# Optimization experiments

Measured on AMD Instinct MI355X. Metric: run time of the kernel, lower is better.

## Reference

```python
import math
import jax, jax.numpy as jnp
import numpy as np

N = 1600; C_IN = 16; HID = 64; OUT = 64; D_K = 8; N_HEADS = 8
CUTS = 8; NUM_RBF = 8; RBF_PROJ = 4; RADIUS = 6.0; ALPHA = 3.0

def leaky(x):
    return jnp.where(x >= 0, x, 0.2 * x)

def group_norm(x, gamma, beta, groups=4, eps=1e-5):
    # x: [N, C]; torch GroupNorm applied on [1, C, N]: stats over (C/groups, N) per group
    n, c = x.shape
    xg = x.T.reshape(groups, -1)
    mu = jnp.mean(xg, axis=1, keepdims=True)
    var = jnp.mean((xg - mu) ** 2, axis=1, keepdims=True)
    xn = ((xg - mu) * jax.lax.rsqrt(var + eps)).reshape(c, n).T
    return xn * gamma + beta

def setup_inputs():
    key = jax.random.key(0)
    ks = jax.random.split(key, 32)
    def rn(k, shape, s=0.1):
        return (jax.random.normal(k, shape) * s).astype(jnp.float32)
    return {
        "points": jax.random.normal(ks[0], (N, 3), jnp.float32),
        "nuv": jax.random.normal(ks[1], (N, 3, 3), jnp.float32),
        "features": jax.random.normal(ks[2], (N, C_IN), jnp.float32),
        "w_in1": rn(ks[3], (HID, C_IN)), "b_in1": rn(ks[4], (HID,)),
        "w_in2": rn(ks[5], (HID, HID)), "b_in2": rn(ks[6], (HID,)),
        "g_in": 1.0 + rn(ks[7], (HID,)), "be_in": rn(ks[8], (HID,)),
        "wq": rn(ks[9], (HID, HID)), "bq": rn(ks[10], (HID,)),
        "wk": rn(ks[11], (HID, HID)), "bk": rn(ks[12], (HID,)),
        "wv": rn(ks[13], (HID, HID)), "bv": rn(ks[14], (HID,)),
        "conv_w1": rn(ks[15], (CUTS, 4 + RBF_PROJ), 0.5),
        "conv_b1": jnp.abs(rn(ks[16], (CUTS,), 0.5)),
        "conv_w2": rn(ks[17], (HID, CUTS), 0.3), "conv_b2": rn(ks[18], (HID,), 0.3),
        "rbf_log_sigma": jnp.log(jnp.asarray(0.6 * 2.0 / (NUM_RBF - 1), jnp.float32)),
        "rbf_a": rn(ks[19], (RBF_PROJ, NUM_RBF), 0.3), "rbf_b": rn(ks[20], (RBF_PROJ,), 0.1),
        "rbf_centers": jnp.linspace(0.0, 2.0, NUM_RBF, dtype=jnp.float32),
        "w_o1": rn(ks[21], (OUT, HID)), "b_o1": rn(ks[22], (OUT,)),
        "w_o2": rn(ks[23], (OUT, OUT)), "b_o2": rn(ks[24], (OUT,)),
        "g_out": 1.0 + rn(ks[25], (OUT,)), "be_out": rn(ks[26], (OUT,)),
        "w_res": rn(ks[27], (OUT, C_IN)), "b_res": rn(ks[28], (OUT,)),
    }

def reference(points, nuv, features, w_in1, b_in1, w_in2, b_in2, g_in, be_in,
              wq, bq, wk, bk, wv, bv, conv_w1, conv_b1, conv_w2, conv_b2,
              rbf_log_sigma, rbf_a, rbf_b, rbf_centers,
              w_o1, b_o1, w_o2, b_o2, g_out, be_out, w_res, b_res):
    # point-wise MLP + GroupNorm
    h = leaky(features @ w_in1.T + b_in1)
    h = leaky(h @ w_in2.T + b_in2)
    h = group_norm(h, g_in, be_in)
    Q = h @ wq.T + bq
    K = h @ wk.T + bk
    V = h @ wv.T + bv
    pts = points / (math.sqrt(2.0) * RADIUS)
    diff = pts[None, :, :] - pts[:, None, :]            # [N, N, 3] = x_j - x_i
    n_i = nuv[:, 0, :]
    n_j = jax.lax.stop_gradient(n_i)                    # j-side normals are detached in the original
    ndot = jnp.einsum("ia,ja->ij", n_i, n_j)            # <n_i, n_j>
    d2 = jnp.sum(diff ** 2, axis=-1) * (2.0 - ndot) ** 2  # pseudo-geodesic squared distance
    W = (1.0 + d2 / ALPHA) ** (-ALPHA)                  # geodesic window weight
    d2_safe = jnp.where(d2 > 0, d2, 1.0)
    base_d = jnp.where(d2 > 0, jnp.sqrt(d2_safe), 0.0)  # safe sqrt (finite grad at 0)
    sigma = jnp.maximum(jnp.exp(rbf_log_sigma), 1e-6)
    R = jnp.exp(-((base_d[:, :, None] - rbf_centers) ** 2) / (2.0 * sigma ** 2))  # [N,N,NUM_RBF]
    R_proj = R @ rbf_a.T + rbf_b                        # [N, N, RBF_PROJ]
    X_loc = jnp.einsum("iab,ijb->ija", nuv, diff)       # local tangent-frame coords [N,N,3]
    X = jnp.concatenate([X_loc, ndot[:, :, None], R_proj], axis=-1)  # [N, N, 4+RBF_PROJ]
    F1 = jax.nn.relu(X @ conv_w1.T + conv_b1)           # shared conv layer-1 [N, N, CUTS]
    scale = 1.0 / math.sqrt(D_K)
    heads = []
    for h_id in range(N_HEADS):
        s = slice(h_id * D_K, (h_id + 1) * D_K)
        Fh = jax.nn.relu(F1 @ conv_w2[s].T + conv_b2[s])      # per-head conv weights [N, N, D_K]
        S = (Q[:, s] @ K[:, s].T) * scale                     # attention logits [N, N]
        P = jax.nn.softmax(S, axis=1) * W                     # softmax over j, fused with window
        heads.append(jnp.einsum("ij,ijc,jc->ic", P, Fh, V[:, s]))
    agg = jnp.concatenate(heads, axis=1)                      # [N, HID]
    o = leaky(agg @ w_o1.T + b_o1)
    o = leaky(o @ w_o2.T + b_o2)
    o = group_norm(o, g_out, be_out)
    return o + features @ w_res.T + b_res
```

## Files before the change

kernel.cpp:

```cpp
#include <hip/hip_runtime.h>

typedef __fp16 h2 __attribute__((ext_vector_type(2)));
typedef unsigned int u32;
typedef unsigned short u16;

#define NPTS 1600
#define NCHUNK 10
#define CHUNKJ 160
#define TILE 32
#define QS (0.35355339059327373f*1.4426950408889634f)
#define PSCALE 0.11785113019775793f
#define LOG2E 1.4426950408889634f

__device__ __forceinline__ float leaky(float x){ return x >= 0.f ? x : 0.2f*x; }
__device__ __forceinline__ float d4(float4 a, float4 b){ return a.x*b.x + a.y*b.y + a.z*b.z + a.w*b.w; }
__device__ __forceinline__ u32 pkn(float a, float b){ h2 v; v[0]=(__fp16)a; v[1]=(__fp16)b; return __builtin_bit_cast(u32,v); }
__device__ __forceinline__ h2 u2h(u32 u){ return __builtin_bit_cast(h2,u); }
__device__ __forceinline__ float dot2(h2 a, h2 b, float c){ return __builtin_amdgcn_fdot2(a,b,c,false); }
__device__ __forceinline__ u32 rfl(u32 x){ return (u32)__builtin_amdgcn_readfirstlane((int)x); }

__global__ __launch_bounds__(256) void k_in(
    const float* __restrict__ feat, const float* __restrict__ w1, const float* __restrict__ b1,
    const float* __restrict__ w2, const float* __restrict__ b2,
    const float* __restrict__ conv_w1, const float* __restrict__ conv_b1,
    const float* __restrict__ conv_w2,
    const float* __restrict__ rbf_a, const float* __restrict__ rbf_b,
    const float* __restrict__ rbf_ls, const float* __restrict__ rbf_c,
    float* __restrict__ h2out, float* __restrict__ bstat1, float* __restrict__ wpk)
{
  __shared__ float sh[4][64];
  __shared__ float sred[4][8];
  int t = threadIdx.x, w = t>>6, c = t&63;
  int i = blockIdx.x*4 + w;

  if (blockIdx.x == 0) {
    u32* wp = (u32*)wpk;
    {
      int row = t>>2, q = t&3;
      wp[32 + row*4 + q] = pkn(conv_w2[row*8+2*q], conv_w2[row*8+2*q+1]);
    }
    if (t < 32) {
      int cc = t>>2, kq = t&3;
      float a0=0.f, a1=0.f;
      #pragma unroll
      for (int p=0;p<4;p++){ a0 += conv_w1[cc*8+4+p]*rbf_a[p*8+2*kq]; a1 += conv_w1[cc*8+4+p]*rbf_a[p*8+2*kq+1]; }
      wp[cc*4+kq] = pkn(a0,a1);
    } else if (t < 40) {
      int cc = t-32; float s = conv_b1[cc];
      #pragma unroll
      for (int p=0;p<4;p++) s += conv_w1[cc*8+4+p]*rbf_b[p];
      wpk[288+cc] = s;
    } else if (t == 40) {
      float sig = fmaxf(expf(rbf_ls[0]), 1e-6f);
      float m = -LOG2E/(2.f*sig*sig);
      float c0 = rbf_c[0];
      float dl = rbf_c[1] - rbf_c[0];
      wpk[296] = c0;
      wpk[297] = m;
      wpk[298] = -2.f*m*dl;
      wpk[299] = m*dl*dl;
    }
  }

  const float4* f4 = (const float4*)(feat + i*16);
  float4 f0=f4[0], f1v=f4[1], f2v=f4[2], f3v=f4[3];
  const float4* w1r = (const float4*)(w1 + c*16);
  float h1 = b1[c] + d4(f0,w1r[0]) + d4(f1v,w1r[1]) + d4(f2v,w1r[2]) + d4(f3v,w1r[3]);
  h1 = leaky(h1);
  sh[w][c] = h1;
  __syncthreads();
  float hh = b2[c];
  #pragma unroll
  for (int k4=0;k4<16;k4++){
    float4 hv = *(const float4*)&sh[w][k4*4];
    hh += d4(hv, *(const float4*)&w2[c*64 + k4*4]);
  }
  hh = leaky(hh);
  h2out[i*64+c] = hh;

  float s = hh, qq = hh*hh;
  s += __shfl_xor(s,1);  qq += __shfl_xor(qq,1);
  s += __shfl_xor(s,2);  qq += __shfl_xor(qq,2);
  s += __shfl_xor(s,4);  qq += __shfl_xor(qq,4);
  s += __shfl_xor(s,8);  qq += __shfl_xor(qq,8);
  if ((c&15)==0){ int g=c>>4; sred[w][g]=s; sred[w][4+g]=qq; }
  __syncthreads();
  if (t<8) bstat1[blockIdx.x*8+t] = sred[0][t]+sred[1][t]+sred[2][t]+sred[3][t];
}

__global__ __launch_bounds__(256) void k_qkv(
  const float* __restrict__ h2b, const float* __restrict__ bstat1,
  const float* __restrict__ g_in, const float* __restrict__ be_in,
  const float* __restrict__ wq, const float* __restrict__ bq,
  const float* __restrict__ wk, const float* __restrict__ bk,
  const float* __restrict__ wv, const float* __restrict__ bv,
  const float* __restrict__ pts, const float* __restrict__ nuv,
  u32* __restrict__ Q16, u32* __restrict__ K16, u32* __restrict__ V16,
  float* __restrict__ PN)
{
  __shared__ float sh[4][64];
  __shared__ float sp[64];
  __shared__ float sst[8];
  int t=threadIdx.x, w=t>>6, c=t&63;
  int i = blockIdx.x*4 + w;
  if (t<64){ int g=t&7; float s=0.f;
    for (int m=t>>3; m<400; m+=8) s += bstat1[m*8+g];
    sp[t]=s; }
  __syncthreads();
  if (t<8){ float s=0.f;
    #pragma unroll
    for (int q=0;q<8;q++) s += sp[q*8+t];
    sst[t]=s; }
  __syncthreads();
  int g = c>>4;
  const float inv = 1.f/25600.f;
  float mu = sst[g]*inv;
  float var = sst[4+g]*inv - mu*mu;
  float rs = rsqrtf(var + 1e-5f);
  float hn = (h2b[i*64+c]-mu)*rs*g_in[c] + be_in[c];
  sh[w][c] = hn;
  __syncthreads();
  float q=bq[c], k=bk[c], v=bv[c];
  #pragma unroll
  for (int k4=0;k4<16;k4++){
    float4 hv = *(const float4*)&sh[w][k4*4];
    q += d4(hv, *(const float4*)&wq[c*64+k4*4]);
    k += d4(hv, *(const float4*)&wk[c*64+k4*4]);
    v += d4(hv, *(const float4*)&wv[c*64+k4*4]);
  }
  u16* Q16u = (u16*)Q16;
  u16* K16u = (u16*)K16;
  u16* V16u = (u16*)V16;
  __fp16 qh = (__fp16)(q*QS);
  __fp16 kh = (__fp16)k;
  __fp16 vh = (__fp16)v;
  Q16u[i*64 + c] = __builtin_bit_cast(u16, qh);
  K16u[i*64 + c] = __builtin_bit_cast(u16, kh);
  int pr = ((i>>5)<<4) + (i&15);
  int hf = (i>>4)&1;
  V16u[(pr*64 + c)*2 + hf] = __builtin_bit_cast(u16, vh);
  if (c < 6){
    float pv = (c<3) ? pts[i*3+c]*PSCALE : nuv[i*9+(c-3)];
    PN[i*8+c] = pv;
  } else if (c < 8) PN[i*8+c] = 0.f;
}

__global__ __launch_bounds__(256) void k_pair(
  const u32* __restrict__ Q16, const u32* __restrict__ K16, const u32* __restrict__ V16,
  const float* __restrict__ PN, const float* __restrict__ nuv,
  const float* __restrict__ w1, const float* __restrict__ wpk,
  const float* __restrict__ b2g, float* __restrict__ part)
{
  __shared__ __align__(16) float SM[4608];
  u32*   sQ16 = (u32*)SM;
  u32*   sWX  = (u32*)SM + 576;
  float* sRed = SM;

  int t = threadIdx.x;
  int r = t & 15, jl = t >> 4;
  int bx = blockIdx.x;
  int rb = bx % 100, jc = bx / 100;
  int I0 = rb*16, J0 = jc*CHUNKJ;
  int i = I0 + r;

  if (t < 128) {
    int qrow = t>>3, qq4 = (t&7)<<2;
    *(uint4*)&sQ16[qrow*36+qq4] = *(const uint4*)&Q16[(I0+qrow)*32+qq4];
  }
  if (t < 128) {
    int r2 = t>>3, cc = t&7, ib = (I0+r2)*9;
    float a0=w1[cc*8], a1=w1[cc*8+1], a2=w1[cc*8+2];
    float x = a0*nuv[ib+0] + a1*nuv[ib+3] + a2*nuv[ib+6];
    float y = a0*nuv[ib+1] + a1*nuv[ib+4] + a2*nuv[ib+7];
    float z = a0*nuv[ib+2] + a1*nuv[ib+5] + a2*nuv[ib+8];
    sWX[r2*20+cc*2+0] = pkn(x,y);
    sWX[r2*20+cc*2+1] = pkn(z, w1[cc*8+3]);
  }
  __syncthreads();
  u32 wxp[16];
  #pragma unroll
  for (int q2=0;q2<4;q2++) *(uint4*)&wxp[q2*4] = *(const uint4*)&sWX[r*20+q2*4];

  const u32* wp = (const u32*)wpk;
  h2 wr[8][4];
  #pragma unroll
  for (int cc=0;cc<8;cc++)
    #pragma unroll
    for (int q2=0;q2<4;q2++) wr[cc][q2] = u2h(rfl(wp[cc*4+q2]));
  const u32* w2p = wp + 32;
  const float* b1p = wpk + 288;
  float c0  = wpk[296];
  float mco = wpk[297];
  float C2  = wpk[298];
  float A1  = wpk[299];

  float4 pni0 = *(const float4*)&PN[i*8];
  float4 pni1 = *(const float4*)&PN[i*8+4];
  float pix = pni0.x, piy = pni0.y, piz = pni0.z;
  float nix = pni0.w, niy = pni1.x, niz = pni1.y;

  float acc[64];
  #pragma unroll
  for (int o=0;o<64;o++) acc[o] = 0.f;
  float lh[8];
  #pragma unroll
  for (int h=0;h<8;h++) lh[h] = 0.f;

  #pragma unroll 1
  for (int tb=0; tb<CHUNKJ; tb+=TILE) {
    int jbase = J0 + tb;
    int jA = jbase + jl;
    int jB = jA + 16;

    h2 F1p[2][4];
    float Wv[2];
    #pragma unroll
    for (int jj=0;jj<2;jj++) {
      int j = jj ? jB : jA;
      float4 a0 = *(const float4*)&PN[j*8];
      float4 a1 = *(const float4*)&PN[j*8+4];
      float dx = a0.x-pix, dy = a0.y-piy, dz = a0.z-piz;
      float ndot = nix*a0.w + niy*a1.x + niz*a1.y;
      float d2r = dx*dx + dy*dy + dz*dz;
      float wf = 2.f - ndot;
      float d2 = d2r*wf*wf;
      float tp = fmaf(d2, 0.3333333333333333f, 1.f);
      Wv[jj] = __builtin_amdgcn_rcpf(tp*tp*tp);
      float dd = __builtin_amdgcn_sqrtf(d2);
      float g0 = dd - c0;
      float s2 = mco*g0*g0;
      float uu = C2*g0;
      float R[8];
      #pragma unroll
      for (int k=0;k<8;k++){
        float kf = (float)k, k2f = (float)(k*k);
        R[k] = __builtin_amdgcn_exp2f(fmaf(kf, uu, fmaf(k2f, A1, s2)));
      }
      h2 xv0; xv0[0]=(__fp16)dx; xv0[1]=(__fp16)dy;
      h2 xv1; xv1[0]=(__fp16)dz; xv1[1]=(__fp16)ndot;
      h2 r01=__builtin_amdgcn_cvt_pkrtz(R[0],R[1]);
      h2 r23=__builtin_amdgcn_cvt_pkrtz(R[2],R[3]);
      h2 r45=__builtin_amdgcn_cvt_pkrtz(R[4],R[5]);
      h2 r67=__builtin_amdgcn_cvt_pkrtz(R[6],R[7]);
      float F1f[8];
      #pragma unroll
      for (int cc=0;cc<8;cc++){
        float f = dot2(r67, wr[cc][3], b1p[cc]);
        f = dot2(r45, wr[cc][2], f);
        f = dot2(r23, wr[cc][1], f);
        f = dot2(r01, wr[cc][0], f);
        f = dot2(u2h(wxp[cc*2+1]), xv1, f);
        f = dot2(u2h(wxp[cc*2+0]), xv0, f);
        F1f[cc] = fmaxf(f, 0.f);
      }
      F1p[jj][0]=__builtin_amdgcn_cvt_pkrtz(F1f[0],F1f[1]);
      F1p[jj][1]=__builtin_amdgcn_cvt_pkrtz(F1f[2],F1f[3]);
      F1p[jj][2]=__builtin_amdgcn_cvt_pkrtz(F1f[4],F1f[5]);
      F1p[jj][3]=__builtin_amdgcn_cvt_pkrtz(F1f[6],F1f[7]);
    }
    h2 Wvp = __builtin_amdgcn_cvt_pkrtz(Wv[0], Wv[1]);

    const u32* kArow = &K16[jA*32];
    const u32* kBrow = &K16[jB*32];
    const u32* vrow  = &V16[(((u32)jbase>>1)+jl)*64];

    #pragma unroll
    for (int h=0;h<8;h++) {
      uint4 qh = *(const uint4*)&sQ16[r*36 + (h<<2)];
      uint4 kA = *(const uint4*)&kArow[h<<2];
      uint4 kB = *(const uint4*)&kBrow[h<<2];
      float S0 = dot2(u2h(qh.x),u2h(kA.x), dot2(u2h(qh.y),u2h(kA.y),
                 dot2(u2h(qh.z),u2h(kA.z), dot2(u2h(qh.w),u2h(kA.w), 0.f))));
      float S1 = dot2(u2h(qh.x),u2h(kB.x), dot2(u2h(qh.y),u2h(kB.y),
                 dot2(u2h(qh.z),u2h(kB.z), dot2(u2h(qh.w),u2h(kB.w), 0.f))));
      float e0 = __builtin_amdgcn_exp2f(S0);
      float e1 = __builtin_amdgcn_exp2f(S1);
      lh[h] += e0 + e1;
      h2 ewp = __builtin_amdgcn_cvt_pkrtz(e0,e1) * Wvp;
      uint4 vpA = *(const uint4*)&vrow[h*8];
      uint4 vpB = *(const uint4*)&vrow[h*8+4];
      u32 vparr[8] = {vpA.x,vpA.y,vpA.z,vpA.w,vpB.x,vpB.y,vpB.z,vpB.w};
      #pragma unroll
      for (int cc=0;cc<8;cc++){
        int rw = h*8+cc;
        h2 w0=u2h(w2p[rw*4+0]), w1h=u2h(w2p[rw*4+1]), w2h=u2h(w2p[rw*4+2]), w3h=u2h(w2p[rw*4+3]);
        float b2v = b2g[rw];
        float fh0 = dot2(F1p[0][0],w0, dot2(F1p[0][1],w1h, dot2(F1p[0][2],w2h, dot2(F1p[0][3],w3h, b2v))));
        float fh1 = dot2(F1p[1][0],w0, dot2(F1p[1][1],w1h, dot2(F1p[1][2],w2h, dot2(F1p[1][3],w3h, b2v))));
        h2 fhp = __builtin_amdgcn_cvt_pkrtz(fmaxf(fh0,0.f), fmaxf(fh1,0.f));
        h2 ev = u2h(vparr[cc]) * ewp;
        acc[rw] = dot2(fhp, ev, acc[rw]);
      }
    }
  }

  #pragma unroll
  for (int o=0;o<64;o++){ acc[o] += __shfl_xor(acc[o],16); acc[o] += __shfl_xor(acc[o],32); }
  #pragma unroll
  for (int h=0;h<8;h++){ lh[h] += __shfl_xor(lh[h],16); lh[h] += __shfl_xor(lh[h],32); }
  __syncthreads();
  int wv = t >> 6, lane = t & 63;
  if (lane < 16) {
    #pragma unroll
    for (int o=0;o<64;o++) sRed[(wv*16+lane)*72+o] = acc[o];
    #pragma unroll
    for (int h=0;h<8;h++) sRed[(wv*16+lane)*72+64+h] = lh[h];
  }
  __syncthreads();
  for (int v2 = t; v2 < 16*72; v2 += 256) {
    int rr = v2/72, o = v2 - rr*72;
    part[(jc*NPTS + I0 + rr)*72 + o] =
      sRed[(0*16+rr)*72+o] + sRed[(1*16+rr)*72+o] + sRed[(2*16+rr)*72+o] + sRed[(3*16+rr)*72+o];
  }
}

__global__ __launch_bounds__(256) void k_agg(
  const float* __restrict__ part, const float* __restrict__ w_o1, const float* __restrict__ b_o1,
  const float* __restrict__ w_o2, const float* __restrict__ b_o2,
  float* __restrict__ o2b, float* __restrict__ bstat2)
{
  __shared__ float sh[4][64];
  __shared__ float sred[4][8];
  int t = threadIdx.x, w = t>>6, c = t&63;
  int i = blockIdx.x*4 + w;
  int h = c>>3;
  float a = 0.f, L = 0.f;
  #pragma unroll
  for (int jc=0;jc<NCHUNK;jc++){
    const float* p = part + (jc*NPTS + i)*72;
    a += p[c]; L += p[64+h];
  }
  float agg = a / L;
  sh[w][c] = agg; __syncthreads();
  float o1 = b_o1[c];
  #pragma unroll
  for (int k4=0;k4<16;k4++){
    float4 hv = *(const float4*)&sh[w][k4*4];
    o1 += d4(hv, *(const float4*)&w_o1[c*64+k4*4]);
  }
  o1 = leaky(o1);
  __syncthreads();
  sh[w][c] = o1; __syncthreads();
  float o2 = b_o2[c];
  #pragma unroll
  for (int k4=0;k4<16;k4++){
    float4 hv = *(const float4*)&sh[w][k4*4];
    o2 += d4(hv, *(const float4*)&w_o2[c*64+k4*4]);
  }
  o2 = leaky(o2);
  o2b[i*64+c] = o2;

  float s = o2, qq = o2*o2;
  s += __shfl_xor(s,1);  qq += __shfl_xor(qq,1);
  s += __shfl_xor(s,2);  qq += __shfl_xor(qq,2);
  s += __shfl_xor(s,4);  qq += __shfl_xor(qq,4);
  s += __shfl_xor(s,8);  qq += __shfl_xor(qq,8);
  if ((c&15)==0){ int g=c>>4; sred[w][g]=s; sred[w][4+g]=qq; }
  __syncthreads();
  if (t<8) bstat2[blockIdx.x*8+t] = sred[0][t]+sred[1][t]+sred[2][t]+sred[3][t];
}

__global__ __launch_bounds__(256) void k_out(
  const float* __restrict__ o2b, const float* __restrict__ bstat2,
  const float* __restrict__ g_out, const float* __restrict__ be_out,
  const float* __restrict__ feat, const float* __restrict__ w_res, const float* __restrict__ b_res,
  float* __restrict__ out)
{
  __shared__ float sp[64];
  __shared__ float sst[8];
  int t = threadIdx.x, w = t>>6, c = t&63;
  int i = blockIdx.x*4 + w;
  if (t<64){ int g=t&7; float s=0.f;
    for (int m=t>>3; m<400; m+=8) s += bstat2[m*8+g];
    sp[t]=s; }
  __syncthreads();
  if (t<8){ float s=0.f;
    #pragma unroll
    for (int q=0;q<8;q++) s += sp[q*8+t];
    sst[t]=s; }
  __syncthreads();
  int g = c>>4;
  const float inv = 1.f/25600.f;
  float mu = sst[g]*inv;
  float var = sst[4+g]*inv - mu*mu;
  float rs = rsqrtf(var + 1e-5f);
  float on = (o2b[i*64+c]-mu)*rs*g_out[c] + be_out[c];
  const float4* f4 = (const float4*)(feat + i*16);
  const float4* wr = (const float4*)(w_res + c*16);
  float res = b_res[c] + d4(f4[0],wr[0]) + d4(f4[1],wr[1]) + d4(f4[2],wr[2]) + d4(f4[3],wr[3]);
  out[i*64+c] = on + res;
}

extern "C" void kernel_launch(void* const* d_in, const int* in_sizes, int n_in,
                              void* d_out, int out_size, void* d_ws, size_t ws_size,
                              hipStream_t stream) {
  const float* points  = (const float*)d_in[0];
  const float* nuv     = (const float*)d_in[1];
  const float* feat    = (const float*)d_in[2];
  const float* w_in1   = (const float*)d_in[3];
  const float* b_in1   = (const float*)d_in[4];
  const float* w_in2   = (const float*)d_in[5];
  const float* b_in2   = (const float*)d_in[6];
  const float* g_in    = (const float*)d_in[7];
  const float* be_in   = (const float*)d_in[8];
  const float* wq      = (const float*)d_in[9];
  const float* bq      = (const float*)d_in[10];
  const float* wk      = (const float*)d_in[11];
  const float* bk      = (const float*)d_in[12];
  const float* wv      = (const float*)d_in[13];
  const float* bv      = (const float*)d_in[14];
  const float* conv_w1 = (const float*)d_in[15];
  const float* conv_b1 = (const float*)d_in[16];
  const float* conv_w2 = (const float*)d_in[17];
  const float* conv_b2 = (const float*)d_in[18];
  const float* rbf_ls  = (const float*)d_in[19];
  const float* rbf_a   = (const float*)d_in[20];
  const float* rbf_b   = (const float*)d_in[21];
  const float* rbf_c   = (const float*)d_in[22];
  const float* w_o1    = (const float*)d_in[23];
  const float* b_o1    = (const float*)d_in[24];
  const float* w_o2    = (const float*)d_in[25];
  const float* b_o2    = (const float*)d_in[26];
  const float* g_out   = (const float*)d_in[27];
  const float* be_out  = (const float*)d_in[28];
  const float* w_res   = (const float*)d_in[29];
  const float* b_res   = (const float*)d_in[30];

  float* ws     = (float*)d_ws;
  float* h2f    = ws;
  u32*   Q16    = (u32*)(ws + 102400);
  u32*   K16    = (u32*)(ws + 153600);
  u32*   V16    = (u32*)(ws + 204800);
  float* PN     = ws + 256000;
  float* bstat1 = ws + 268800;
  float* bstat2 = ws + 272000;
  float* wpk    = ws + 275200;
  float* part   = ws + 275520;
  float* o2b    = ws + 1427520;
  float* out    = (float*)d_out;

  k_in<<<400, 256, 0, stream>>>(feat, w_in1, b_in1, w_in2, b_in2,
                                conv_w1, conv_b1, conv_w2, rbf_a, rbf_b, rbf_ls, rbf_c,
                                h2f, bstat1, wpk);
  k_qkv<<<400, 256, 0, stream>>>(h2f, bstat1, g_in, be_in, wq, bq, wk, bk, wv, bv,
                                 points, nuv, Q16, K16, V16, PN);
  k_pair<<<1000, 256, 0, stream>>>(Q16, K16, V16, PN, nuv, conv_w1, wpk, conv_b2, part);
  k_agg<<<400, 256, 0, stream>>>(part, w_o1, b_o1, w_o2, b_o2, o2b, bstat2);
  k_out<<<400, 256, 0, stream>>>(o2b, bstat2, g_out, be_out, feat, w_res, b_res, out);
}
```

Before: 238.1 us.

## Split pair kernel into two head-halves and compute RBF by recurrence

The pair kernel now processes heads in two passes of four, halving the per-thread accumulator array to cut register pressure and raise occupancy. The cost is recomputing the geometric and conv layer-1 features for each pass. The eight RBF exponentials are replaced by two exp2 calls plus a multiplicative recurrence, using constants precomputed in the setup kernel. Dot-product chains are split into parallel partial sums for more instruction-level parallelism, and the WX weights are read from shared memory instead of being held in registers.

```diff
diff --git a/kernel.cpp b/kernel.cpp
--- a/kernel.cpp
+++ b/kernel.cpp
@@ -55,10 +55,14 @@
       float m = -LOG2E/(2.f*sig*sig);
       float c0 = rbf_c[0];
       float dl = rbf_c[1] - rbf_c[0];
+      float A1v = m*dl*dl;
       wpk[296] = c0;
       wpk[297] = m;
       wpk[298] = -2.f*m*dl;
-      wpk[299] = m*dl*dl;
+      wpk[299] = A1v;
+      float Av = exp2f(A1v);
+      wpk[300] = Av;
+      wpk[301] = Av*Av;
     }
   }
 
@@ -151,10 +155,9 @@
   const float* __restrict__ w1, const float* __restrict__ wpk,
   const float* __restrict__ b2g, float* __restrict__ part)
 {
-  __shared__ __align__(16) float SM[4608];
-  u32*   sQ16 = (u32*)SM;
-  u32*   sWX  = (u32*)SM + 576;
-  float* sRed = SM;
+  __shared__ __align__(16) u32   sQ16[16*36];
+  __shared__ __align__(16) u32   sWX[16*20];
+  __shared__ __align__(16) float sRedH[4*16*36];
 
   int t = threadIdx.x;
   int r = t & 15, jl = t >> 4;
@@ -177,9 +180,6 @@
     sWX[r2*20+cc*2+1] = pkn(z, w1[cc*8+3]);
   }
   __syncthreads();
-  u32 wxp[16];
-  #pragma unroll
-  for (int q2=0;q2<4;q2++) *(uint4*)&wxp[q2*4] = *(const uint4*)&sWX[r*20+q2*4];
 
   const u32* wp = (const u32*)wpk;
   h2 wr[8][4];
@@ -192,125 +192,128 @@
   float c0  = wpk[296];
   float mco = wpk[297];
   float C2  = wpk[298];
-  float A1  = wpk[299];
+  float Af  = wpk[300];
+  float A2f = wpk[301];
 
   float4 pni0 = *(const float4*)&PN[i*8];
   float4 pni1 = *(const float4*)&PN[i*8+4];
   float pix = pni0.x, piy = pni0.y, piz = pni0.z;
   float nix = pni0.w, niy = pni1.x, niz = pni1.y;
 
-  float acc[64];
-  #pragma unroll
-  for (int o=0;o<64;o++) acc[o] = 0.f;
-  float lh[8];
-  #pragma unroll
-  for (int h=0;h<8;h++) lh[h] = 0.f;
-
   #pragma unroll 1
-  for (int tb=0; tb<CHUNKJ; tb+=TILE) {
-    int jbase = J0 + tb;
-    int jA = jbase + jl;
-    int jB = jA + 16;
-
-    h2 F1p[2][4];
-    float Wv[2];
-    #pragma unroll
-    for (int jj=0;jj<2;jj++) {
-      int j = jj ? jB : jA;
-      float4 a0 = *(const float4*)&PN[j*8];
-      float4 a1 = *(const float4*)&PN[j*8+4];
-      float dx = a0.x-pix, dy = a0.y-piy, dz = a0.z-piz;
-      float ndot = nix*a0.w + niy*a1.x + niz*a1.y;
-      float d2r = dx*dx + dy*dy + dz*dz;
-      float wf = 2.f - ndot;
-      float d2 = d2r*wf*wf;
-      float tp = fmaf(d2, 0.3333333333333333f, 1.f);
-      Wv[jj] = __builtin_amdgcn_rcpf(tp*tp*tp);
-      float dd = __builtin_amdgcn_sqrtf(d2);
-      float g0 = dd - c0;
-      float s2 = mco*g0*g0;
-      float uu = C2*g0;
-      float R[8];
-      #pragma unroll
-      for (int k=0;k<8;k++){
-        float kf = (float)k, k2f = (float)(k*k);
-        R[k] = __builtin_amdgcn_exp2f(fmaf(kf, uu, fmaf(k2f, A1, s2)));
+  for (int hp=0; hp<2; hp++) {
+    float acc[32];
+    #pragma unroll
+    for (int o=0;o<32;o++) acc[o] = 0.f;
+    float lh[4] = {0.f,0.f,0.f,0.f};
+
+    #pragma unroll 1
+    for (int tb=0; tb<CHUNKJ; tb+=TILE) {
+      int jbase = J0 + tb;
+      int jA = jbase + jl;
+      int jB = jA + 16;
+
+      h2 F1p[2][4];
+      float Wv[2];
+      #pragma unroll
+      for (int jj=0;jj<2;jj++) {
+        int j = jj ? jB : jA;
+        float4 a0 = *(const float4*)&PN[j*8];
+        float4 a1 = *(const float4*)&PN[j*8+4];
+        float dx = a0.x-pix, dy = a0.y-piy, dz = a0.z-piz;
+        float ndot = nix*a0.w + niy*a1.x + niz*a1.y;
+        float d2r = dx*dx + dy*dy + dz*dz;
+        float wf = 2.f - ndot;
+        float d2 = d2r*wf*wf;
+        float tp = fmaf(d2, 0.3333333333333333f, 1.f);
+        Wv[jj] = __builtin_amdgcn_rcpf(tp*tp*tp);
+        float dd = __builtin_amdgcn_sqrtf(d2);
+        float g0 = dd - c0;
+        float E = __builtin_amdgcn_exp2f(mco*g0*g0);
+        float U = __builtin_amdgcn_exp2f(C2*g0);
+        float R[8];
+        R[0] = E;
+        float tt = U*Af;
+        #pragma unroll
+        for (int k=1;k<8;k++){ R[k] = R[k-1]*tt; tt *= A2f; }
+        h2 xv0; xv0[0]=(__fp16)dx; xv0[1]=(__fp16)dy;
+        h2 xv1; xv1[0]=(__fp16)dz; xv1[1]=(__fp16)ndot;
+        h2 r01=__builtin_amdgcn_cvt_pkrtz(R[0],R[1]);
+        h2 r23=__builtin_amdgcn_cvt_pkrtz(R[2],R[3]);
+        h2 r45=__builtin_amdgcn_cvt_pkrtz(R[4],R[5]);
+        h2 r67=__builtin_amdgcn_cvt_pkrtz(R[6],R[7]);
+        float F1f[8];
+        #pragma unroll
+        for (int cc=0;cc<8;cc++){
+          uint2 wx2 = *(const uint2*)&sWX[r*20+cc*2];
+          float fa = dot2(r01, wr[cc][0], dot2(r23, wr[cc][1], b1p[cc]));
+          float fb = dot2(r45, wr[cc][2], dot2(r67, wr[cc][3], 0.f));
+          float fc = dot2(u2h(wx2.x), xv0, dot2(u2h(wx2.y), xv1, 0.f));
+          F1f[cc] = fmaxf(fa+fb+fc, 0.f);
+        }
+        F1p[jj][0]=__builtin_amdgcn_cvt_pkrtz(F1f[0],F1f[1]);
+        F1p[jj][1]=__builtin_amdgcn_cvt_pkrtz(F1f[2],F1f[3]);
+        F1p[jj][2]=__builtin_amdgcn_cvt_pkrtz(F1f[4],F1f[5]);
+        F1p[jj][3]=__builtin_amdgcn_cvt_pkrtz(F1f[6],F1f[7]);
       }
-      h2 xv0; xv0[0]=(__fp16)dx; xv0[1]=(__fp16)dy;
-      h2 xv1; xv1[0]=(__fp16)dz; xv1[1]=(__fp16)ndot;
-      h2 r01=__builtin_amdgcn_cvt_pkrtz(R[0],R[1]);
-      h2 r23=__builtin_amdgcn_cvt_pkrtz(R[2],R[3]);
-      h2 r45=__builtin_amdgcn_cvt_pkrtz(R[4],R[5]);
-      h2 r67=__builtin_amdgcn_cvt_pkrtz(R[6],R[7]);
-      float F1f[8];
-      #pragma unroll
-      for (int cc=0;cc<8;cc++){
-        float f = dot2(r67, wr[cc][3], b1p[cc]);
-        f = dot2(r45, wr[cc][2], f);
-        f = dot2(r23, wr[cc][1], f);
-        f = dot2(r01, wr[cc][0], f);
-        f = dot2(u2h(wxp[cc*2+1]), xv1, f);
-        f = dot2(u2h(wxp[cc*2+0]), xv0, f);
-        F1f[cc] = fmaxf(f, 0.f);
-      }
-      F1p[jj][0]=__builtin_amdgcn_cvt_pkrtz(F1f[0],F1f[1]);
-      F1p[jj][1]=__builtin_amdgcn_cvt_pkrtz(F1f[2],F1f[3]);
-      F1p[jj][2]=__builtin_amdgcn_cvt_pkrtz(F1f[4],F1f[5]);
-      F1p[jj][3]=__builtin_amdgcn_cvt_pkrtz(F1f[6],F1f[7]);
-    }
-    h2 Wvp = __builtin_amdgcn_cvt_pkrtz(Wv[0], Wv[1]);
-
-    const u32* kArow = &K16[jA*32];
-    const u32* kBrow = &K16[jB*32];
-    const u32* vrow  = &V16[(((u32)jbase>>1)+jl)*64];
-
-    #pragma unroll
-    for (int h=0;h<8;h++) {
-      uint4 qh = *(const uint4*)&sQ16[r*36 + (h<<2)];
-      uint4 kA = *(const uint4*)&kArow[h<<2];
-      uint4 kB = *(const uint4*)&kBrow[h<<2];
-      float S0 = dot2(u2h(qh.x),u2h(kA.x), dot2(u2h(qh.y),u2h(kA.y),
-                 dot2(u2h(qh.z),u2h(kA.z), dot2(u2h(qh.w),u2h(kA.w), 0.f))));
-      float S1 = dot2(u2h(qh.x),u2h(kB.x), dot2(u2h(qh.y),u2h(kB.y),
-                 dot2(u2h(qh.z),u2h(kB.z), dot2(u2h(qh.w),u2h(kB.w), 0.f))));
-      float e0 = __builtin_amdgcn_exp2f(S0);
-      float e1 = __builtin_amdgcn_exp2f(S1);
-      lh[h] += e0 + e1;
-      h2 ewp = __builtin_amdgcn_cvt_pkrtz(e0,e1) * Wvp;
-      uint4 vpA = *(const uint4*)&vrow[h*8];
-      uint4 vpB = *(const uint4*)&vrow[h*8+4];
-      u32 vparr[8] = {vpA.x,vpA.y,vpA.z,vpA.w,vpB.x,vpB.y,vpB.z,vpB.w};
-      #pragma unroll
-      for (int cc=0;cc<8;cc++){
-        int rw = h*8+cc;
-        h2 w0=u2h(w2p[rw*4+0]), w1h=u2h(w2p[rw*4+1]), w2h=u2h(w2p[rw*4+2]), w3h=u2h(w2p[rw*4+3]);
-        float b2v = b2g[rw];
-        float fh0 = dot2(F1p[0][0],w0, dot2(F1p[0][1],w1h, dot2(F1p[0][2],w2h, dot2(F1p[0][3],w3h, b2v))));
-        float fh1 = dot2(F1p[1][0],w0, dot2(F1p[1][1],w1h, dot2(F1p[1][2],w2h, dot2(F1p[1][3],w3h, b2v))));
-        h2 fhp = __builtin_amdgcn_cvt_pkrtz(fmaxf(fh0,0.f), fmaxf(fh1,0.f));
-        h2 ev = u2h(vparr[cc]) * ewp;
-        acc[rw] = dot2(fhp, ev, acc[rw]);
+      h2 Wvp = __builtin_amdgcn_cvt_pkrtz(Wv[0], Wv[1]);
+
+      const u32* kArow = &K16[jA*32];
+      const u32* kBrow = &K16[jB*32];
+      const u32* vrow  = &V16[(((u32)jbase>>1)+jl)*64];
+
+      #pragma unroll
+      for (int hh=0; hh<4; hh++) {
+        int h = (hp<<2) + hh;
+        uint4 qh = *(const uint4*)&sQ16[r*36 + (h<<2)];
+        uint4 kA = *(const uint4*)&kArow[h<<2];
+        uint4 kB = *(const uint4*)&kBrow[h<<2];
+        float S0 = dot2(u2h(qh.x),u2h(kA.x), dot2(u2h(qh.y),u2h(kA.y), 0.f))
+                 + dot2(u2h(qh.z),u2h(kA.z), dot2(u2h(qh.w),u2h(kA.w), 0.f));
+        float S1 = dot2(u2h(qh.x),u2h(kB.x), dot2(u2h(qh.y),u2h(kB.y), 0.f))
+                 + dot2(u2h(qh.z),u2h(kB.z), dot2(u2h(qh.w),u2h(kB.w), 0.f));
+        float e0 = __builtin_amdgcn_exp2f(S0);
+        float e1 = __builtin_amdgcn_exp2f(S1);
+        lh[hh] += e0 + e1;
+        h2 ewp = __builtin_amdgcn_cvt_pkrtz(e0,e1) * Wvp;
+        uint4 vpA = *(const uint4*)&vrow[h*8];
+        uint4 vpB = *(const uint4*)&vrow[h*8+4];
+        u32 vparr[8] = {vpA.x,vpA.y,vpA.z,vpA.w,vpB.x,vpB.y,vpB.z,vpB.w};
+        #pragma unroll
+        for (int cc=0;cc<8;cc++){
+          int rw = h*8+cc;
+          h2 w0=u2h(w2p[rw*4+0]), w1h=u2h(w2p[rw*4+1]), w2h=u2h(w2p[rw*4+2]), w3h=u2h(w2p[rw*4+3]);
+          float b2v = b2g[rw];
+          float fh0 = dot2(F1p[0][0],w0, dot2(F1p[0][1],w1h, b2v))
+                    + dot2(F1p[0][2],w2h, dot2(F1p[0][3],w3h, 0.f));
+          float fh1 = dot2(F1p[1][0],w0, dot2(F1p[1][1],w1h, b2v))
+                    + dot2(F1p[1][2],w2h, dot2(F1p[1][3],w3h, 0.f));
+          h2 fhp = __builtin_amdgcn_cvt_pkrtz(fmaxf(fh0,0.f), fmaxf(fh1,0.f));
+          h2 ev = u2h(vparr[cc]) * ewp;
+          acc[hh*8+cc] = dot2(fhp, ev, acc[hh*8+cc]);
+        }
       }
     }
-  }
-
-  #pragma unroll
-  for (int o=0;o<64;o++){ acc[o] += __shfl_xor(acc[o],16); acc[o] += __shfl_xor(acc[o],32); }
-  #pragma unroll
-  for (int h=0;h<8;h++){ lh[h] += __shfl_xor(lh[h],16); lh[h] += __shfl_xor(lh[h],32); }
-  __syncthreads();
-  int wv = t >> 6, lane = t & 63;
-  if (lane < 16) {
-    #pragma unroll
-    for (int o=0;o<64;o++) sRed[(wv*16+lane)*72+o] = acc[o];
-    #pragma unroll
-    for (int h=0;h<8;h++) sRed[(wv*16+lane)*72+64+h] = lh[h];
-  }
-  __syncthreads();
-  for (int v2 = t; v2 < 16*72; v2 += 256) {
-    int rr = v2/72, o = v2 - rr*72;
-    part[(jc*NPTS + I0 + rr)*72 + o] =
-      sRed[(0*16+rr)*72+o] + sRed[(1*16+rr)*72+o] + sRed[(2*16+rr)*72+o] + sRed[(3*16+rr)*72+o];
+
+    #pragma unroll
+    for (int o=0;o<32;o++){ acc[o] += __shfl_xor(acc[o],16); acc[o] += __shfl_xor(acc[o],32); }
+    #pragma unroll
+    for (int hh=0;hh<4;hh++){ lh[hh] += __shfl_xor(lh[hh],16); lh[hh] += __shfl_xor(lh[hh],32); }
+    __syncthreads();
+    int wv = t >> 6, lane = t & 63;
+    if (lane < 16) {
+      #pragma unroll
+      for (int o=0;o<32;o++) sRedH[(wv*16+lane)*36+o] = acc[o];
+      #pragma unroll
+      for (int hh=0;hh<4;hh++) sRedH[(wv*16+lane)*36+32+hh] = lh[hh];
+    }
+    __syncthreads();
+    for (int v2 = t; v2 < 16*36; v2 += 256) {
+      int rr = v2/36, o = v2 - rr*36;
+      float s = sRedH[(0*16+rr)*36+o]+sRedH[(1*16+rr)*36+o]+sRedH[(2*16+rr)*36+o]+sRedH[(3*16+rr)*36+o];
+      int off = (o < 32) ? (hp<<5)+o : 64 + (hp<<2) + (o-32);
+      part[(jc*NPTS + I0 + rr)*72 + off] = s;
+    }
   }
 }
 
```

Result: slower. 262.9 us (+10.4%).
